# Optimization experiments

Hardware: AMD Instinct MI355X
Metric: run time of the kernel (lower is better)

Reference implementation:

```python
import jax, jax.numpy as jnp
import numpy as np

D = 512            # model size
H = 8              # num_heads
HD = D // H        # head_size = 64
WIN = 7            # num_keys (payload tokens per window)
QNB = 5            # query_nb for 'mean' aggregation
SCALE = D ** -0.5  # NOTE: torch module scales by size**-0.5, not head_size**-0.5
EPS = 1e-5


def setup_inputs() -> dict:
    key = jax.random.key(0)
    ks = jax.random.split(key, 12)
    B, M = 8, 4096
    w = lambda i: jax.random.normal(ks[i], (D, D), jnp.float32) * 0.02
    return {
        "k": jax.random.normal(ks[0], (B, M, D), jnp.float32),
        "v": jax.random.normal(ks[1], (B, M, D), jnp.float32),
        "q": jax.random.normal(ks[2], (B, M, D), jnp.float32),
        "query_len": 3584,
        "Wk": w(3), "bk": jnp.zeros((D,), jnp.float32),
        "Wv": w(4), "bv": jnp.zeros((D,), jnp.float32),
        "Wq": w(5), "bq": jnp.zeros((D,), jnp.float32),
        "ln_g": jnp.ones((D,), jnp.float32), "ln_b": jnp.zeros((D,), jnp.float32),
        "Wpq": w(6), "bpq": jnp.zeros((D,), jnp.float32),
        "Wpk": w(7), "bpk": jnp.zeros((D,), jnp.float32),
        "Wo": w(8), "bo": jnp.zeros((D,), jnp.float32),
    }


def reference(k, v, q, query_len, Wk, bk, Wv, bv, Wq, bq, ln_g, ln_b, Wpq, bpq, Wpk, bpk, Wo, bo):
    B, M, _ = k.shape
    win_num = -(-query_len // WIN)     # ceil
    per_win = M // win_num

    k = k @ Wk + bk
    v = v @ Wv + bv
    q = q @ Wq + bq

    # 'mean' query aggregation: AvgPool1d(kernel=QNB, stride=1, pad=QNB//2),
    # count_include_pad=True => always divide by QNB (zero-padded)
    qp = jnp.pad(q, ((0, 0), (QNB // 2, QNB // 2), (0, 0)))
    q = sum(qp[:, j:j + M] for j in range(QNB)) / QNB

    # ---- stage 1: DSA (local attention inside each window of per_win tokens)
    resh = lambda x: x.reshape(B, win_num, per_win, H, HD).transpose(0, 1, 3, 2, 4)
    dq, dk, dv = resh(q), resh(k), resh(v)                       # [B,W,H,p,hd]
    attn = jax.nn.softmax(jnp.einsum('bwhqd,bwhkd->bwhqk', dq, dk) * SCALE, axis=-1)
    out = jnp.einsum('bwhqk,bwhkd->bwhqd', attn, dv)
    out = out.transpose(0, 1, 3, 2, 4).reshape(B, win_num, per_win, D)

    win_tok = out[:, :, 0, :]          # [B, W, D] window summary tokens
    attn_x = out[:, :, 1:, :]

    # LayerNorm + exact GELU on window tokens
    mu = win_tok.mean(-1, keepdims=True)
    var = ((win_tok - mu) ** 2).mean(-1, keepdims=True)
    win_tok = (win_tok - mu) / jnp.sqrt(var + EPS) * ln_g + ln_b
    win_tok = jax.nn.gelu(win_tok, approximate=False)

    # ---- stage 2: PSA (attention over window summary tokens)
    pq = (win_tok @ Wpq + bpq).reshape(B, win_num, H, HD).transpose(0, 2, 1, 3)  # [B,H,W,hd]
    pk = (win_tok @ Wpk + bpk).reshape(B, win_num, H, HD).transpose(0, 2, 1, 3)
    pv = attn_x.reshape(B, win_num, WIN, H, HD).transpose(0, 3, 1, 2, 4)
    pv = pv.reshape(B, H, win_num, WIN * HD)

    pattn = jax.nn.softmax(jnp.einsum('bhqd,bhkd->bhqk', pq, pk) * SCALE, axis=-1)
    pout = jnp.einsum('bhqk,bhkd->bhqd', pattn, pv)
    pout = pout.transpose(0, 2, 1, 3).reshape(B, win_num, H, WIN, HD)
    pout = pout.transpose(0, 1, 3, 2, 4).reshape(B, win_num, WIN, D)

    out = (pout + attn_x).reshape(B, win_num * WIN, D)[:, :query_len, :]
    return out @ Wo + bo
```

## Files before the change

### kernel.cpp

```cpp
#include <hip/hip_runtime.h>
#include <hip/hip_bf16.h>
#include <math.h>

#define SCALE_ 0.04419417382415922f
#define EPS_  1e-5f

typedef unsigned short u16;
typedef __attribute__((ext_vector_type(8))) short     bf16x8;
typedef __attribute__((ext_vector_type(4))) float     f32x4;
typedef __attribute__((ext_vector_type(8))) unsigned short u16x8;
typedef __attribute__((ext_vector_type(4))) unsigned short u16x4;

__device__ __forceinline__ u16 f2b(float f) {
  union { float f; unsigned int u; } x; x.f = f;
  unsigned int u = x.u;
  return (u16)((u + 0x7FFFu + ((u >> 16) & 1u)) >> 16);
}
__device__ __forceinline__ float b2f(u16 h) {
  union { unsigned int u; float f; } x; x.u = ((unsigned int)h) << 16;
  return x.f;
}
__device__ __forceinline__ void gload_lds16(const void* g, void* l) {
  __builtin_amdgcn_global_load_lds(
      (const __attribute__((address_space(1))) void*)g,
      (__attribute__((address_space(3))) void*)l, 16, 0, 0);
}

__global__ __launch_bounds__(256) void wconv(
    const float* W0, const float* W1, const float* W2,
    const float* W3, const float* W4, const float* W5, u16* wt)
{
  const float* W;
  switch (blockIdx.z) {
    case 0: W = W0; break; case 1: W = W1; break; case 2: W = W2; break;
    case 3: W = W3; break; case 4: W = W4; break; default: W = W5; break;
  }
  u16* Wt = wt + (size_t)blockIdx.z * 262144;
  const int k0 = blockIdx.x * 64, n0 = blockIdx.y * 64;
  __shared__ float T[64][68];
  const int tid = threadIdx.x;
#pragma unroll
  for (int it = 0; it < 4; ++it) {
    int L = it * 256 + tid;
    int r = L >> 4, cg = L & 15;
    float4 v = *reinterpret_cast<const float4*>(W + (size_t)(k0 + r) * 512 + n0 + cg * 4);
    T[r][cg * 4 + 0] = v.x; T[r][cg * 4 + 1] = v.y;
    T[r][cg * 4 + 2] = v.z; T[r][cg * 4 + 3] = v.w;
  }
  __syncthreads();
#pragma unroll
  for (int it = 0; it < 2; ++it) {
    int L = it * 256 + tid;
    int rn = L >> 3, kg = L & 7;
    u16x8 o;
#pragma unroll
    for (int e = 0; e < 8; ++e) o[e] = f2b(T[kg * 8 + e][rn]);
    *(u16x8*)(Wt + (size_t)(n0 + rn) * 512 + k0 + kg * 8) = o;
  }
}

__global__ __launch_bounds__(512) void gemm_proj(
    const float* A0, const u16* Bt0, const float* bi0, u16* C0,
    const float* A1, const u16* Bt1, const float* bi1, u16* C1,
    const float* A2, const u16* Bt2, const float* bi2, u16* C2)
{
  const float *A, *bias; const u16* Bt; u16* C;
  if (blockIdx.z == 0)      { A = A0; Bt = Bt0; bias = bi0; C = C0; }
  else if (blockIdx.z == 1) { A = A1; Bt = Bt1; bias = bi1; C = C1; }
  else                      { A = A2; Bt = Bt2; bias = bi2; C = C2; }

  __shared__ u16 As[8192];
  __shared__ u16 Bs[32768];
  const int tid = threadIdx.x;
  const int lane = tid & 63, wid = tid >> 6;
  const int wr = wid >> 2, wcn = wid & 3;
  const int l15 = lane & 15, lh = lane >> 4, l7 = lane & 7;
  const int m0 = blockIdx.x * 128;

  const f32x4 fz = {0.f, 0.f, 0.f, 0.f};
  f32x4 acc[4][8];
#pragma unroll
  for (int m = 0; m < 4; ++m)
#pragma unroll
    for (int n = 0; n < 8; ++n) acc[m][n] = fz;

  int aoff[2], boff[2];
#pragma unroll
  for (int kh = 0; kh < 2; ++kh) {
    int slot = ((kh * 4 + lh) ^ l7) << 4;
    aoff[kh] = (wr * 64 + l15) * 128 + slot;
    boff[kh] = (wcn * 128 + l15) * 128 + slot;
  }

  for (int k0 = 0; k0 < 512; k0 += 64) {
    __syncthreads();
#pragma unroll
    for (int it = 0; it < 8; ++it) {
      int L = it * 512 + tid;
      int r = L >> 3, s = L & 7;
      int c = s ^ (r & 7);
      gload_lds16(Bt + (size_t)r * 512 + k0 + c * 8,
                  (char*)Bs + (it * 512 + wid * 64) * 16);
    }
    float4 xa[2], xb[2];
#pragma unroll
    for (int it = 0; it < 2; ++it) {
      int L = it * 512 + tid;
      int r = L >> 3, s = L & 7;
      int c = s ^ (r & 7);
      const float* ga = A + (size_t)(m0 + r) * 512 + k0 + c * 8;
      xa[it] = *reinterpret_cast<const float4*>(ga);
      xb[it] = *reinterpret_cast<const float4*>(ga + 4);
    }
#pragma unroll
    for (int it = 0; it < 2; ++it) {
      int L = it * 512 + tid;
      u16x8 o;
      o[0] = f2b(xa[it].x); o[1] = f2b(xa[it].y);
      o[2] = f2b(xa[it].z); o[3] = f2b(xa[it].w);
      o[4] = f2b(xb[it].x); o[5] = f2b(xb[it].y);
      o[6] = f2b(xb[it].z); o[7] = f2b(xb[it].w);
      *(u16x8*)((char*)As + L * 16) = o;
    }
    __syncthreads();
#pragma unroll
    for (int kh = 0; kh < 2; ++kh) {
      bf16x8 af[4], bfr[8];
#pragma unroll
      for (int m = 0; m < 4; ++m)
        af[m] = *(const bf16x8*)((const char*)As + aoff[kh] + m * 2048);
#pragma unroll
      for (int n = 0; n < 8; ++n)
        bfr[n] = *(const bf16x8*)((const char*)Bs + boff[kh] + n * 2048);
#pragma unroll
      for (int m = 0; m < 4; ++m)
#pragma unroll
        for (int n = 0; n < 8; ++n)
          acc[m][n] = __builtin_amdgcn_mfma_f32_16x16x32_bf16(af[m], bfr[n], acc[m][n], 0, 0, 0);
    }
  }

  const int gn0 = wcn * 128 + l15;
  float bv[8];
#pragma unroll
  for (int n = 0; n < 8; ++n) bv[n] = bias[gn0 + n * 16];
#pragma unroll
  for (int m = 0; m < 4; ++m)
#pragma unroll
    for (int reg = 0; reg < 4; ++reg) {
      int gm = m0 + wr * 64 + m * 16 + lh * 4 + reg;
#pragma unroll
      for (int n = 0; n < 8; ++n)
        C[(size_t)gm * 512 + gn0 + n * 16] = f2b(acc[m][n][reg] + bv[n]);
    }
}

__global__ __launch_bounds__(512) void gemm_out(
    const u16* __restrict__ A, const u16* __restrict__ Bt,
    const float* __restrict__ bias, float* __restrict__ C)
{
  __shared__ u16 As[8192];
  __shared__ u16 Bs[32768];
  const int tid = threadIdx.x;
  const int lane = tid & 63, wid = tid >> 6;
  const int wr = wid >> 2, wcn = wid & 3;
  const int l15 = lane & 15, lh = lane >> 4, l7 = lane & 7;
  const int m0 = blockIdx.x * 128;

  const f32x4 fz = {0.f, 0.f, 0.f, 0.f};
  f32x4 acc[4][8];
#pragma unroll
  for (int m = 0; m < 4; ++m)
#pragma unroll
    for (int n = 0; n < 8; ++n) acc[m][n] = fz;

  int aoff[2], boff[2];
#pragma unroll
  for (int kh = 0; kh < 2; ++kh) {
    int slot = ((kh * 4 + lh) ^ l7) << 4;
    aoff[kh] = (wr * 64 + l15) * 128 + slot;
    boff[kh] = (wcn * 128 + l15) * 128 + slot;
  }

  for (int k0 = 0; k0 < 512; k0 += 64) {
    __syncthreads();
#pragma unroll
    for (int it = 0; it < 8; ++it) {
      int L = it * 512 + tid;
      int r = L >> 3, s = L & 7;
      int c = s ^ (r & 7);
      gload_lds16(Bt + (size_t)r * 512 + k0 + c * 8,
                  (char*)Bs + (it * 512 + wid * 64) * 16);
    }
#pragma unroll
    for (int it = 0; it < 2; ++it) {
      int L = it * 512 + tid;
      int r = L >> 3, s = L & 7;
      int c = s ^ (r & 7);
      gload_lds16(A + (size_t)(m0 + r) * 512 + k0 + c * 8,
                  (char*)As + (it * 512 + wid * 64) * 16);
    }
    __syncthreads();
#pragma unroll
    for (int kh = 0; kh < 2; ++kh) {
      bf16x8 af[4], bfr[8];
#pragma unroll
      for (int m = 0; m < 4; ++m)
        af[m] = *(const bf16x8*)((const char*)As + aoff[kh] + m * 2048);
#pragma unroll
      for (int n = 0; n < 8; ++n)
        bfr[n] = *(const bf16x8*)((const char*)Bs + boff[kh] + n * 2048);
#pragma unroll
      for (int m = 0; m < 4; ++m)
#pragma unroll
        for (int n = 0; n < 8; ++n)
          acc[m][n] = __builtin_amdgcn_mfma_f32_16x16x32_bf16(af[m], bfr[n], acc[m][n], 0, 0, 0);
    }
  }

  const int gn0 = wcn * 128 + l15;
  float bv[8];
#pragma unroll
  for (int n = 0; n < 8; ++n) bv[n] = bias[gn0 + n * 16];
#pragma unroll
  for (int m = 0; m < 4; ++m)
#pragma unroll
    for (int reg = 0; reg < 4; ++reg) {
      int gm = m0 + wr * 64 + m * 16 + lh * 4 + reg;
#pragma unroll
      for (int n = 0; n < 8; ++n)
        C[(size_t)gm * 512 + gn0 + n * 16] = acc[m][n][reg] + bv[n];
    }
}

__global__ __launch_bounds__(256) void gemm_pp(
    const u16* __restrict__ A,
    const u16* __restrict__ Bt0, const float* __restrict__ bi0, float* __restrict__ C0,
    const u16* __restrict__ Bt1, const float* __restrict__ bi1, float* __restrict__ C1)
{
  const u16* Bt; const float* bias; float* C;
  if (blockIdx.z == 0) { Bt = Bt0; bias = bi0; C = C0; }
  else                 { Bt = Bt1; bias = bi1; C = C1; }

  __shared__ u16 As[8192];
  __shared__ u16 Bs[8192];
  const int tid = threadIdx.x;
  const int lane = tid & 63, wid = tid >> 6;
  const int wr = wid >> 1, wc = wid & 1;
  const int l15 = lane & 15, lh = lane >> 4, l7 = lane & 7;
  const int m0 = blockIdx.x * 128, n0 = blockIdx.y * 128;

  const f32x4 fz = {0.f, 0.f, 0.f, 0.f};
  f32x4 acc[4][4];
#pragma unroll
  for (int m = 0; m < 4; ++m)
#pragma unroll
    for (int n = 0; n < 4; ++n) acc[m][n] = fz;

  int aoff[2], boff[2];
#pragma unroll
  for (int kh = 0; kh < 2; ++kh) {
    int slot = ((kh * 4 + lh) ^ l7) << 4;
    aoff[kh] = (wr * 64 + l15) * 128 + slot;
    boff[kh] = (wc * 64 + l15) * 128 + slot;
  }

  for (int k0 = 0; k0 < 512; k0 += 64) {
    __syncthreads();
#pragma unroll
    for (int it = 0; it < 4; ++it) {
      int L = it * 256 + tid;
      int r = L >> 3, s = L & 7;
      int c = s ^ (r & 7);
      gload_lds16(A  + (size_t)(m0 + r) * 512 + k0 + c * 8,
                  (char*)As + (it * 256 + wid * 64) * 16);
      gload_lds16(Bt + (size_t)(n0 + r) * 512 + k0 + c * 8,
                  (char*)Bs + (it * 256 + wid * 64) * 16);
    }
    __syncthreads();
#pragma unroll
    for (int kh = 0; kh < 2; ++kh) {
      bf16x8 af[4], bfr[4];
#pragma unroll
      for (int m = 0; m < 4; ++m)
        af[m] = *(const bf16x8*)((const char*)As + aoff[kh] + m * 2048);
#pragma unroll
      for (int n = 0; n < 4; ++n)
        bfr[n] = *(const bf16x8*)((const char*)Bs + boff[kh] + n * 2048);
#pragma unroll
      for (int m = 0; m < 4; ++m)
#pragma unroll
        for (int n = 0; n < 4; ++n)
          acc[m][n] = __builtin_amdgcn_mfma_f32_16x16x32_bf16(af[m], bfr[n], acc[m][n], 0, 0, 0);
    }
  }

  const int gn0 = n0 + wc * 64 + l15;
  float bv[4];
#pragma unroll
  for (int n = 0; n < 4; ++n) bv[n] = bias[gn0 + n * 16];
#pragma unroll
  for (int m = 0; m < 4; ++m)
#pragma unroll
    for (int reg = 0; reg < 4; ++reg) {
      int gm = m0 + wr * 64 + m * 16 + lh * 4 + reg;
#pragma unroll
      for (int n = 0; n < 4; ++n)
        C[(size_t)gm * 512 + gn0 + n * 16] = acc[m][n][reg] + bv[n];
    }
}

__global__ __launch_bounds__(64) void attn_win(
    const u16* kp, const u16* vp, const u16* qp0, u16* attn)
{
  const int h = blockIdx.x, w = blockIdx.y, b = blockIdx.z;
  const int t = threadIdx.x;
  __shared__ float ks[8][68], vs[8][68], qr[12][68], qs[8][68], Ps[8][9];
  const size_t base = ((size_t)b * 4096 + (size_t)w * 8) * 512 + h * 64;

  {
    int i = t >> 3, dg = t & 7;
    u16x8 kv = *(const u16x8*)(kp + base + (size_t)i * 512 + dg * 8);
    u16x8 vv = *(const u16x8*)(vp + base + (size_t)i * 512 + dg * 8);
#pragma unroll
    for (int e = 0; e < 8; ++e) {
      ks[i][dg * 8 + e] = b2f(kv[e]);
      vs[i][dg * 8 + e] = b2f(vv[e]);
    }
  }
#pragma unroll
  for (int l = 0; l < 2; ++l) {
    int L = t + l * 64;
    if (L < 96) {
      int i = L >> 3, dg = L & 7;
      int m = w * 8 - 2 + i;
      if (m >= 0 && m < 4096) {
        u16x8 qv = *(const u16x8*)(qp0 + ((size_t)b * 4096 + m) * 512 + h * 64 + dg * 8);
#pragma unroll
        for (int e = 0; e < 8; ++e) qr[i][dg * 8 + e] = b2f(qv[e]);
      } else {
#pragma unroll
        for (int e = 0; e < 8; ++e) qr[i][dg * 8 + e] = 0.0f;
      }
    }
  }
  __syncthreads();
#pragma unroll
  for (int j = 0; j < 8; ++j)
    qs[j][t] = 0.2f * (qr[j][t] + qr[j + 1][t] + qr[j + 2][t] + qr[j + 3][t] + qr[j + 4][t]);
  __syncthreads();

  const int qi = t >> 3, kj = t & 7;
  float s = 0.0f;
#pragma unroll
  for (int d = 0; d < 64; ++d) s = fmaf(qs[qi][d], ks[kj][d], s);
  s *= SCALE_;
  float mx = s;
  mx = fmaxf(mx, __shfl_xor(mx, 1));
  mx = fmaxf(mx, __shfl_xor(mx, 2));
  mx = fmaxf(mx, __shfl_xor(mx, 4));
  float e = expf(s - mx);
  float sum = e;
  sum += __shfl_xor(sum, 1);
  sum += __shfl_xor(sum, 2);
  sum += __shfl_xor(sum, 4);
  Ps[qi][kj] = e / sum;
  __syncthreads();

  float o[8];
#pragma unroll
  for (int c = 0; c < 8; ++c) o[c] = 0.0f;
#pragma unroll
  for (int tt = 0; tt < 8; ++tt) {
    float pw = Ps[qi][tt];
#pragma unroll
    for (int c = 0; c < 8; ++c) o[c] = fmaf(pw, vs[tt][kj * 8 + c], o[c]);
  }
  u16x8 ov;
#pragma unroll
  for (int c = 0; c < 8; ++c) ov[c] = f2b(o[c]);
  *(u16x8*)(attn + base + (size_t)qi * 512 + kj * 8) = ov;
}

__global__ __launch_bounds__(256) void pvt_build(const u16* attn, u16* pvT)
{
  const int bh = blockIdx.x;
  const int b = bh >> 3, h = bh & 7;
  const int w0 = blockIdx.y * 32;
  __shared__ u16 TL[448 * 40];
  const int tid = threadIdx.x;
#pragma unroll
  for (int it = 0; it < 8; ++it) {
    int L = it * 256 + tid;
    int dg = L & 7, r = L >> 3;
    int w2l = r >> 3, tt = r & 7;
    if (tt < 7) {
      int m = 8 * (w0 + w2l) + tt + 1;
      u16x8 v = *(const u16x8*)(attn + ((size_t)b * 4096 + m) * 512 + h * 64 + dg * 8);
#pragma unroll
      for (int e = 0; e < 8; ++e)
        TL[(tt * 64 + dg * 8 + e) * 40 + w2l] = v[e];
    }
  }
  __syncthreads();
#pragma unroll
  for (int it = 0; it < 7; ++it) {
    int L = it * 256 + tid;
    int n = L >> 2, seg = L & 3;
    u16x8 v = *(const u16x8*)(&TL[n * 40 + seg * 8]);
    *(u16x8*)(pvT + ((size_t)bh * 448 + n) * 512 + w0 + seg * 8) = v;
  }
}

__global__ __launch_bounds__(64) void ln_gelu(
    const u16* attn, const float* g, const float* be, u16* wt)
{
  const int r = blockIdx.x;
  const int b = r >> 9, w = r & 511;
  const int t = threadIdx.x;
  const u16* x = attn + (((size_t)b * 4096) + (size_t)w * 8) * 512;

  u16x8 v = *(const u16x8*)(x + t * 8);
  float xv[8];
  float s1 = 0.f, s2 = 0.f;
#pragma unroll
  for (int e = 0; e < 8; ++e) {
    xv[e] = b2f(v[e]);
    s1 += xv[e]; s2 += xv[e] * xv[e];
  }
#pragma unroll
  for (int off = 1; off < 64; off <<= 1) {
    s1 += __shfl_xor(s1, off);
    s2 += __shfl_xor(s2, off);
  }
  const float mu  = s1 * (1.0f / 512.0f);
  const float var = s2 * (1.0f / 512.0f) - mu * mu;
  const float inv = 1.0f / sqrtf(var + EPS_);

  const int d0 = t * 8;
  float4 g0 = *reinterpret_cast<const float4*>(g + d0);
  float4 g1 = *reinterpret_cast<const float4*>(g + d0 + 4);
  float4 b0 = *reinterpret_cast<const float4*>(be + d0);
  float4 b1 = *reinterpret_cast<const float4*>(be + d0 + 4);
  float gv[8] = {g0.x, g0.y, g0.z, g0.w, g1.x, g1.y, g1.z, g1.w};
  float bvv[8] = {b0.x, b0.y, b0.z, b0.w, b1.x, b1.y, b1.z, b1.w};
  const float k2 = 0.70710678118654752f;
  u16x8 ov;
#pragma unroll
  for (int e = 0; e < 8; ++e) {
    float y = (xv[e] - mu) * inv * gv[e] + bvv[e];
    ov[e] = f2b(0.5f * y * (1.0f + erff(y * k2)));
  }
  *(u16x8*)(wt + (size_t)r * 512 + d0) = ov;
}

__global__ __launch_bounds__(256) void qk_exp(
    const float* pq, const float* pk, u16* expS)
{
  const int bh = blockIdx.z;
  const int b = bh >> 3, h = bh & 7;
  const int wq0 = blockIdx.x * 64, wk0 = blockIdx.y * 64;
  const int tid = threadIdx.x;

  __shared__ float Aq[64][68];
  __shared__ float Bk[64][68];

#pragma unroll
  for (int l = 0; l < 4; ++l) {
    int L = tid + l * 256;
    int row = L >> 4, dv = L & 15;
    float4 a = *reinterpret_cast<const float4*>(pq + ((size_t)b * 512 + wq0 + row) * 512 + h * 64 + dv * 4);
    float4 c = *reinterpret_cast<const float4*>(pk + ((size_t)b * 512 + wk0 + row) * 512 + h * 64 + dv * 4);
    Aq[dv * 4 + 0][row] = a.x; Aq[dv * 4 + 1][row] = a.y;
    Aq[dv * 4 + 2][row] = a.z; Aq[dv * 4 + 3][row] = a.w;
    Bk[dv * 4 + 0][row] = c.x; Bk[dv * 4 + 1][row] = c.y;
    Bk[dv * 4 + 2][row] = c.z; Bk[dv * 4 + 3][row] = c.w;
  }
  __syncthreads();

  const int r0 = (tid >> 4) * 4, c0 = (tid & 15) * 4;
  float acc[4][4];
#pragma unroll
  for (int i = 0; i < 4; ++i)
#pragma unroll
    for (int j = 0; j < 4; ++j) acc[i][j] = 0.0f;

#pragma unroll
  for (int kk = 0; kk < 64; ++kk) {
    float4 a = *reinterpret_cast<const float4*>(&Aq[kk][r0]);
    float4 c = *reinterpret_cast<const float4*>(&Bk[kk][c0]);
    float av[4] = {a.x, a.y, a.z, a.w};
    float cv[4] = {c.x, c.y, c.z, c.w};
#pragma unroll
    for (int i = 0; i < 4; ++i)
#pragma unroll
      for (int j = 0; j < 4; ++j)
        acc[i][j] = fmaf(av[i], cv[j], acc[i][j]);
  }

#pragma unroll
  for (int i = 0; i < 4; ++i) {
    u16x4 o;
#pragma unroll
    for (int j = 0; j < 4; ++j) o[j] = f2b(expf(acc[i][j] * SCALE_));
    *(u16x4*)(expS + ((size_t)bh * 512 + wq0 + r0 + i) * 512 + wk0 + c0) = o;
  }
}

__global__ __launch_bounds__(256) void rs_inv(const u16* expS, float* rsinv)
{
  const int row = blockIdx.x * 4 + (threadIdx.x >> 6);
  const int t = threadIdx.x & 63;
  u16x8 v = *(const u16x8*)(expS + (size_t)row * 512 + t * 8);
  float s = 0.f;
#pragma unroll
  for (int e = 0; e < 8; ++e) s += b2f(v[e]);
#pragma unroll
  for (int off = 1; off < 64; off <<= 1) s += __shfl_xor(s, off);
  if (t == 0) rsinv[row] = 1.0f / s;
}

__global__ __launch_bounds__(256) void pv_mfma(
    const u16* __restrict__ expS, const u16* __restrict__ pvT,
    const float* __restrict__ rsinv, const u16* __restrict__ attn,
    u16* __restrict__ X2)
{
  __shared__ u16 As[8192];
  __shared__ u16 Bs[4096];
  const int tid = threadIdx.x;
  const int lane = tid & 63, wid = tid >> 6;
  const int wr = wid >> 1, wc = wid & 1;
  const int l15 = lane & 15, lh = lane >> 4, l7 = lane & 7;
  const int bh = blockIdx.z, b = bh >> 3, h = bh & 7;
  const int m0 = blockIdx.x * 128;
  const int nt = blockIdx.y;

  const f32x4 fz = {0.f, 0.f, 0.f, 0.f};
  f32x4 acc[4][2];
#pragma unroll
  for (int m = 0; m < 4; ++m)
#pragma unroll
    for (int n = 0; n < 2; ++n) acc[m][n] = fz;

  int aoff[2], boff[2];
#pragma unroll
  for (int kh = 0; kh < 2; ++kh) {
    int slot = ((kh * 4 + lh) ^ l7) << 4;
    aoff[kh] = (wr * 64 + l15) * 128 + slot;
    boff[kh] = (wc * 32 + l15) * 128 + slot;
  }

  for (int k0 = 0; k0 < 512; k0 += 64) {
    __syncthreads();
#pragma unroll
    for (int it = 0; it < 4; ++it) {
      int L = it * 256 + tid;
      int r = L >> 3, s = L & 7;
      int c = s ^ (r & 7);
      gload_lds16(expS + ((size_t)bh * 512 + m0 + r) * 512 + k0 + c * 8,
                  (char*)As + (it * 256 + wid * 64) * 16);
    }
#pragma unroll
    for (int it = 0; it < 2; ++it) {
      int L = it * 256 + tid;
      int r = L >> 3, s = L & 7;
      int c = s ^ (r & 7);
      gload_lds16(pvT + ((size_t)bh * 448 + nt * 64 + r) * 512 + k0 + c * 8,
                  (char*)Bs + (it * 256 + wid * 64) * 16);
    }
    __syncthreads();
#pragma unroll
    for (int kh = 0; kh < 2; ++kh) {
      bf16x8 af[4], bfr[2];
#pragma unroll
      for (int m = 0; m < 4; ++m)
        af[m] = *(const bf16x8*)((const char*)As + aoff[kh] + m * 2048);
#pragma unroll
      for (int n = 0; n < 2; ++n)
        bfr[n] = *(const bf16x8*)((const char*)Bs + boff[kh] + n * 2048);
#pragma unroll
      for (int m = 0; m < 4; ++m)
#pragma unroll
        for (int n = 0; n < 2; ++n)
          acc[m][n] = __builtin_amdgcn_mfma_f32_16x16x32_bf16(af[m], bfr[n], acc[m][n], 0, 0, 0);
    }
  }

#pragma unroll
  for (int m = 0; m < 4; ++m)
#pragma unroll
    for (int reg = 0; reg < 4; ++reg) {
      int gm = m0 + wr * 64 + m * 16 + lh * 4 + reg;
      float ri = rsinv[bh * 512 + gm];
#pragma unroll
      for (int n = 0; n < 2; ++n) {
        int d = wc * 32 + n * 16 + l15;
        float res = b2f(attn[((size_t)b * 4096 + gm * 8 + nt + 1) * 512 + h * 64 + d]);
        X2[((size_t)b * 3584 + gm * 7 + nt) * 512 + h * 64 + d] =
            f2b(acc[m][n][reg] * ri + res);
      }
    }
}

extern "C" void kernel_launch(void* const* d_in, const int* in_sizes, int n_in,
                              void* d_out, int out_size, void* d_ws, size_t ws_size,
                              hipStream_t stream)
{
  const float* k_in = (const float*)d_in[0];
  const float* v_in = (const float*)d_in[1];
  const float* q_in = (const float*)d_in[2];
  const float* Wk  = (const float*)d_in[4];
  const float* bk  = (const float*)d_in[5];
  const float* Wv  = (const float*)d_in[6];
  const float* bv  = (const float*)d_in[7];
  const float* Wq  = (const float*)d_in[8];
  const float* bq  = (const float*)d_in[9];
  const float* lng = (const float*)d_in[10];
  const float* lnb = (const float*)d_in[11];
  const float* Wpq = (const float*)d_in[12];
  const float* bpq = (const float*)d_in[13];
  const float* Wpk = (const float*)d_in[14];
  const float* bpk = (const float*)d_in[15];
  const float* Wo  = (const float*)d_in[16];
  const float* bo  = (const float*)d_in[17];
  float* out = (float*)d_out;

  char* ws = (char*)d_ws;
  const size_t MB = 1024 * 1024;
  u16* wtb  = (u16*)(ws);
  u16* kp   = (u16*)(ws + 16 * MB);
  u16* vp   = (u16*)(ws + 52 * MB);
  u16* qp0  = (u16*)(ws + 88 * MB);
  u16* attn = (u16*)(ws + 124 * MB);
  u16*   wt    = (u16*)(ws + 16 * MB);
  float* pq    = (float*)(ws + 20 * MB);
  float* pk    = (float*)(ws + 28 * MB);
  float* rsinv = (float*)(ws + 36 * MB);
  u16*   expS  = (u16*)(ws + 40 * MB);
  u16*   pvT   = (u16*)(ws + 76 * MB);
  u16*   X2    = (u16*)(ws + 160 * MB);

  u16* Wkt  = wtb;
  u16* Wvt  = wtb + 1 * 262144;
  u16* Wqt  = wtb + 2 * 262144;
  u16* Wpqt = wtb + 3 * 262144;
  u16* Wpkt = wtb + 4 * 262144;
  u16* Wot  = wtb + 5 * 262144;

  wconv<<<dim3(8, 8, 6), 256, 0, stream>>>(Wk, Wv, Wq, Wpq, Wpk, Wo, wtb);

  gemm_proj<<<dim3(256, 1, 3), 512, 0, stream>>>(
      k_in, Wkt, bk, kp,
      v_in, Wvt, bv, vp,
      q_in, Wqt, bq, qp0);

  attn_win<<<dim3(8, 512, 8), 64, 0, stream>>>(kp, vp, qp0, attn);
  pvt_build<<<dim3(64, 16), 256, 0, stream>>>(attn, pvT);
  ln_gelu<<<4096, 64, 0, stream>>>(attn, lng, lnb, wt);

  gemm_pp<<<dim3(32, 4, 2), 256, 0, stream>>>(
      wt, Wpqt, bpq, pq, Wpkt, bpk, pk);

  qk_exp<<<dim3(8, 8, 64), 256, 0, stream>>>(pq, pk, expS);
  rs_inv<<<8192, 256, 0, stream>>>(expS, rsinv);
  pv_mfma<<<dim3(4, 7, 64), 256, 0, stream>>>(expS, pvT, rsinv, attn, X2);

  gemm_out<<<dim3(224, 1, 1), 512, 0, stream>>>(X2, Wot, bo, out);
}
```

Baseline: 301.3 us.

## Double-buffer projection GEMMs and move PSA QK scores onto bf16 MFMA

The projection and output GEMMs now use K-steps of 32 with two LDS buffers, so the global loads for the next step are issued before the MFMAs on the current step, and a new XOR swizzle suits the 64-byte rows. gemm_pp now writes pq and pk in bf16. The scalar fp32 qk_exp kernel is replaced by qk_mfma, which loads them with global-to-LDS copies and computes scores with bf16 MFMA. This is meant to hide memory latency in the big GEMMs and move the PSA score computation onto the matrix cores, at the cost of bf16 rounding on the query and key projections.

New measurement: 281.1 us. -6.7%, faster.

```diff
diff --git a/kernel.cpp b/kernel.cpp
--- a/kernel.cpp
+++ b/kernel.cpp
@@ -69,13 +69,17 @@
   else if (blockIdx.z == 1) { A = A1; Bt = Bt1; bias = bi1; C = C1; }
   else                      { A = A2; Bt = Bt2; bias = bi2; C = C2; }
 
-  __shared__ u16 As[8192];
-  __shared__ u16 Bs[32768];
+  __shared__ u16 As[2][4096];
+  __shared__ u16 Bs[2][16384];
   const int tid = threadIdx.x;
   const int lane = tid & 63, wid = tid >> 6;
   const int wr = wid >> 2, wcn = wid & 3;
-  const int l15 = lane & 15, lh = lane >> 4, l7 = lane & 7;
+  const int l15 = lane & 15, lh = lane >> 4;
+  const int sx = (l15 >> 1) & 3;
   const int m0 = blockIdx.x * 128;
+
+  const int rr = tid >> 2, sp = tid & 3;
+  const int ssw = sp ^ ((rr >> 1) & 3);
 
   const f32x4 fz = {0.f, 0.f, 0.f, 0.f};
   f32x4 acc[4][8];
@@ -84,60 +88,57 @@
 #pragma unroll
     for (int n = 0; n < 8; ++n) acc[m][n] = fz;
 
-  int aoff[2], boff[2];
-#pragma unroll
-  for (int kh = 0; kh < 2; ++kh) {
-    int slot = ((kh * 4 + lh) ^ l7) << 4;
-    aoff[kh] = (wr * 64 + l15) * 128 + slot;
-    boff[kh] = (wcn * 128 + l15) * 128 + slot;
-  }
-
-  for (int k0 = 0; k0 < 512; k0 += 64) {
+  const int aoff0 = (wr * 64 + l15) * 64 + ((lh ^ sx) << 4);
+  const int boff0 = (wcn * 128 + l15) * 64 + ((lh ^ sx) << 4);
+
+  {
+#pragma unroll
+    for (int it = 0; it < 4; ++it)
+      gload_lds16(Bt + (size_t)(it * 128 + rr) * 512 + ssw * 8,
+                  (char*)Bs[0] + (it * 512 + wid * 64) * 16);
+    const float* ga = A + (size_t)(m0 + rr) * 512 + ssw * 8;
+    float4 x0 = *reinterpret_cast<const float4*>(ga);
+    float4 x1 = *reinterpret_cast<const float4*>(ga + 4);
+    u16x8 o;
+    o[0] = f2b(x0.x); o[1] = f2b(x0.y); o[2] = f2b(x0.z); o[3] = f2b(x0.w);
+    o[4] = f2b(x1.x); o[5] = f2b(x1.y); o[6] = f2b(x1.z); o[7] = f2b(x1.w);
+    *(u16x8*)((char*)As[0] + tid * 16) = o;
+  }
+  __syncthreads();
+
+#pragma unroll 2
+  for (int t = 0; t < 16; ++t) {
+    const int cur = t & 1, nxt = cur ^ 1;
+    float4 x0 = {0.f,0.f,0.f,0.f}, x1 = {0.f,0.f,0.f,0.f};
+    if (t < 15) {
+      const int k0 = (t + 1) * 32;
+#pragma unroll
+      for (int it = 0; it < 4; ++it)
+        gload_lds16(Bt + (size_t)(it * 128 + rr) * 512 + k0 + ssw * 8,
+                    (char*)Bs[nxt] + (it * 512 + wid * 64) * 16);
+      const float* ga = A + (size_t)(m0 + rr) * 512 + k0 + ssw * 8;
+      x0 = *reinterpret_cast<const float4*>(ga);
+      x1 = *reinterpret_cast<const float4*>(ga + 4);
+    }
+    bf16x8 af[4], bfr[8];
+#pragma unroll
+    for (int m = 0; m < 4; ++m)
+      af[m] = *(const bf16x8*)((const char*)As[cur] + aoff0 + m * 1024);
+#pragma unroll
+    for (int n = 0; n < 8; ++n)
+      bfr[n] = *(const bf16x8*)((const char*)Bs[cur] + boff0 + n * 1024);
+#pragma unroll
+    for (int m = 0; m < 4; ++m)
+#pragma unroll
+      for (int n = 0; n < 8; ++n)
+        acc[m][n] = __builtin_amdgcn_mfma_f32_16x16x32_bf16(af[m], bfr[n], acc[m][n], 0, 0, 0);
+    if (t < 15) {
+      u16x8 o;
+      o[0] = f2b(x0.x); o[1] = f2b(x0.y); o[2] = f2b(x0.z); o[3] = f2b(x0.w);
+      o[4] = f2b(x1.x); o[5] = f2b(x1.y); o[6] = f2b(x1.z); o[7] = f2b(x1.w);
+      *(u16x8*)((char*)As[nxt] + tid * 16) = o;
+    }
     __syncthreads();
-#pragma unroll
-    for (int it = 0; it < 8; ++it) {
-      int L = it * 512 + tid;
-      int r = L >> 3, s = L & 7;
-      int c = s ^ (r & 7);
-      gload_lds16(Bt + (size_t)r * 512 + k0 + c * 8,
-                  (char*)Bs + (it * 512 + wid * 64) * 16);
-    }
-    float4 xa[2], xb[2];
-#pragma unroll
-    for (int it = 0; it < 2; ++it) {
-      int L = it * 512 + tid;
-      int r = L >> 3, s = L & 7;
-      int c = s ^ (r & 7);
-      const float* ga = A + (size_t)(m0 + r) * 512 + k0 + c * 8;
-      xa[it] = *reinterpret_cast<const float4*>(ga);
-      xb[it] = *reinterpret_cast<const float4*>(ga + 4);
-    }
-#pragma unroll
-    for (int it = 0; it < 2; ++it) {
-      int L = it * 512 + tid;
-      u16x8 o;
-      o[0] = f2b(xa[it].x); o[1] = f2b(xa[it].y);
-      o[2] = f2b(xa[it].z); o[3] = f2b(xa[it].w);
-      o[4] = f2b(xb[it].x); o[5] = f2b(xb[it].y);
-      o[6] = f2b(xb[it].z); o[7] = f2b(xb[it].w);
-      *(u16x8*)((char*)As + L * 16) = o;
-    }
-    __syncthreads();
-#pragma unroll
-    for (int kh = 0; kh < 2; ++kh) {
-      bf16x8 af[4], bfr[8];
-#pragma unroll
-      for (int m = 0; m < 4; ++m)
-        af[m] = *(const bf16x8*)((const char*)As + aoff[kh] + m * 2048);
-#pragma unroll
-      for (int n = 0; n < 8; ++n)
-        bfr[n] = *(const bf16x8*)((const char*)Bs + boff[kh] + n * 2048);
-#pragma unroll
-      for (int m = 0; m < 4; ++m)
-#pragma unroll
-        for (int n = 0; n < 8; ++n)
-          acc[m][n] = __builtin_amdgcn_mfma_f32_16x16x32_bf16(af[m], bfr[n], acc[m][n], 0, 0, 0);
-    }
   }
 
   const int gn0 = wcn * 128 + l15;
@@ -159,13 +160,16 @@
     const u16* __restrict__ A, const u16* __restrict__ Bt,
     const float* __restrict__ bias, float* __restrict__ C)
 {
-  __shared__ u16 As[8192];
-  __shared__ u16 Bs[32768];
+  __shared__ u16 As[2][4096];
+  __shared__ u16 Bs[2][16384];
   const int tid = threadIdx.x;
   const int lane = tid & 63, wid = tid >> 6;
   const int wr = wid >> 2, wcn = wid & 3;
-  const int l15 = lane & 15, lh = lane >> 4, l7 = lane & 7;
+  const int l15 = lane & 15, lh = lane >> 4;
+  const int sx = (l15 >> 1) & 3;
   const int m0 = blockIdx.x * 128;
+  const int rr = tid >> 2, sp = tid & 3;
+  const int ssw = sp ^ ((rr >> 1) & 3);
 
   const f32x4 fz = {0.f, 0.f, 0.f, 0.f};
   f32x4 acc[4][8];
@@ -174,48 +178,44 @@
 #pragma unroll
     for (int n = 0; n < 8; ++n) acc[m][n] = fz;
 
-  int aoff[2], boff[2];
-#pragma unroll
-  for (int kh = 0; kh < 2; ++kh) {
-    int slot = ((kh * 4 + lh) ^ l7) << 4;
-    aoff[kh] = (wr * 64 + l15) * 128 + slot;
-    boff[kh] = (wcn * 128 + l15) * 128 + slot;
-  }
-
-  for (int k0 = 0; k0 < 512; k0 += 64) {
+  const int aoff0 = (wr * 64 + l15) * 64 + ((lh ^ sx) << 4);
+  const int boff0 = (wcn * 128 + l15) * 64 + ((lh ^ sx) << 4);
+
+  {
+#pragma unroll
+    for (int it = 0; it < 4; ++it)
+      gload_lds16(Bt + (size_t)(it * 128 + rr) * 512 + ssw * 8,
+                  (char*)Bs[0] + (it * 512 + wid * 64) * 16);
+    gload_lds16(A + (size_t)(m0 + rr) * 512 + ssw * 8,
+                (char*)As[0] + (wid * 64) * 16);
+  }
+  __syncthreads();
+
+#pragma unroll 2
+  for (int t = 0; t < 16; ++t) {
+    const int cur = t & 1, nxt = cur ^ 1;
+    if (t < 15) {
+      const int k0 = (t + 1) * 32;
+#pragma unroll
+      for (int it = 0; it < 4; ++it)
+        gload_lds16(Bt + (size_t)(it * 128 + rr) * 512 + k0 + ssw * 8,
+                    (char*)Bs[nxt] + (it * 512 + wid * 64) * 16);
+      gload_lds16(A + (size_t)(m0 + rr) * 512 + k0 + ssw * 8,
+                  (char*)As[nxt] + (wid * 64) * 16);
+    }
+    bf16x8 af[4], bfr[8];
+#pragma unroll
+    for (int m = 0; m < 4; ++m)
+      af[m] = *(const bf16x8*)((const char*)As[cur] + aoff0 + m * 1024);
+#pragma unroll
+    for (int n = 0; n < 8; ++n)
+      bfr[n] = *(const bf16x8*)((const char*)Bs[cur] + boff0 + n * 1024);
+#pragma unroll
+    for (int m = 0; m < 4; ++m)
+#pragma unroll
+      for (int n = 0; n < 8; ++n)
+        acc[m][n] = __builtin_amdgcn_mfma_f32_16x16x32_bf16(af[m], bfr[n], acc[m][n], 0, 0, 0);
     __syncthreads();
-#pragma unroll
-    for (int it = 0; it < 8; ++it) {
-      int L = it * 512 + tid;
-      int r = L >> 3, s = L & 7;
-      int c = s ^ (r & 7);
-      gload_lds16(Bt + (size_t)r * 512 + k0 + c * 8,
-                  (char*)Bs + (it * 512 + wid * 64) * 16);
-    }
-#pragma unroll
-    for (int it = 0; it < 2; ++it) {
-      int L = it * 512 + tid;
-      int r = L >> 3, s = L & 7;
-      int c = s ^ (r & 7);
-      gload_lds16(A + (size_t)(m0 + r) * 512 + k0 + c * 8,
-                  (char*)As + (it * 512 + wid * 64) * 16);
-    }
-    __syncthreads();
-#pragma unroll
-    for (int kh = 0; kh < 2; ++kh) {
-      bf16x8 af[4], bfr[8];
-#pragma unroll
-      for (int m = 0; m < 4; ++m)
-        af[m] = *(const bf16x8*)((const char*)As + aoff[kh] + m * 2048);
-#pragma unroll
-      for (int n = 0; n < 8; ++n)
-        bfr[n] = *(const bf16x8*)((const char*)Bs + boff[kh] + n * 2048);
-#pragma unroll
-      for (int m = 0; m < 4; ++m)
-#pragma unroll
-        for (int n = 0; n < 8; ++n)
-          acc[m][n] = __builtin_amdgcn_mfma_f32_16x16x32_bf16(af[m], bfr[n], acc[m][n], 0, 0, 0);
-    }
   }
 
   const int gn0 = wcn * 128 + l15;
@@ -235,10 +235,10 @@
 
 __global__ __launch_bounds__(256) void gemm_pp(
     const u16* __restrict__ A,
-    const u16* __restrict__ Bt0, const float* __restrict__ bi0, float* __restrict__ C0,
-    const u16* __restrict__ Bt1, const float* __restrict__ bi1, float* __restrict__ C1)
-{
-  const u16* Bt; const float* bias; float* C;
+    const u16* __restrict__ Bt0, const float* __restrict__ bi0, u16* __restrict__ C0,
+    const u16* __restrict__ Bt1, const float* __restrict__ bi1, u16* __restrict__ C1)
+{
+  const u16* Bt; const float* bias; u16* C;
   if (blockIdx.z == 0) { Bt = Bt0; bias = bi0; C = C0; }
   else                 { Bt = Bt1; bias = bi1; C = C1; }
 
@@ -306,7 +306,70 @@
       int gm = m0 + wr * 64 + m * 16 + lh * 4 + reg;
 #pragma unroll
       for (int n = 0; n < 4; ++n)
-        C[(size_t)gm * 512 + gn0 + n * 16] = acc[m][n][reg] + bv[n];
+        C[(size_t)gm * 512 + gn0 + n * 16] = f2b(acc[m][n][reg] + bv[n]);
+    }
+}
+
+__global__ __launch_bounds__(256) void qk_mfma(
+    const u16* __restrict__ pq, const u16* __restrict__ pk, u16* __restrict__ expS)
+{
+  __shared__ u16 As[8192];
+  __shared__ u16 Bs[8192];
+  const int tid = threadIdx.x;
+  const int lane = tid & 63, wid = tid >> 6;
+  const int wr = wid >> 1, wc = wid & 1;
+  const int l15 = lane & 15, lh = lane >> 4, l7 = lane & 7;
+  const int bh = blockIdx.z, b = bh >> 3, h = bh & 7;
+  const int wq0 = blockIdx.x * 128, wk0 = blockIdx.y * 128;
+
+  const f32x4 fz = {0.f, 0.f, 0.f, 0.f};
+  f32x4 acc[4][4];
+#pragma unroll
+  for (int m = 0; m < 4; ++m)
+#pragma unroll
+    for (int n = 0; n < 4; ++n) acc[m][n] = fz;
+
+#pragma unroll
+  for (int it = 0; it < 4; ++it) {
+    int L = it * 256 + tid;
+    int r = L >> 3, s = L & 7;
+    int c = s ^ (r & 7);
+    gload_lds16(pq + ((size_t)b * 512 + wq0 + r) * 512 + h * 64 + c * 8,
+                (char*)As + (it * 256 + wid * 64) * 16);
+    gload_lds16(pk + ((size_t)b * 512 + wk0 + r) * 512 + h * 64 + c * 8,
+                (char*)Bs + (it * 256 + wid * 64) * 16);
+  }
+  __syncthreads();
+
+#pragma unroll
+  for (int kh = 0; kh < 2; ++kh) {
+    int slot = ((kh * 4 + lh) ^ l7) << 4;
+    int aoff = (wr * 64 + l15) * 128 + slot;
+    int boff = (wc * 64 + l15) * 128 + slot;
+    bf16x8 af[4], bfr[4];
+#pragma unroll
+    for (int m = 0; m < 4; ++m)
+      af[m] = *(const bf16x8*)((const char*)As + aoff + m * 2048);
+#pragma unroll
+    for (int n = 0; n < 4; ++n)
+      bfr[n] = *(const bf16x8*)((const char*)Bs + boff + n * 2048);
+#pragma unroll
+    for (int m = 0; m < 4; ++m)
+#pragma unroll
+      for (int n = 0; n < 4; ++n)
+        acc[m][n] = __builtin_amdgcn_mfma_f32_16x16x32_bf16(af[m], bfr[n], acc[m][n], 0, 0, 0);
+  }
+
+  const int gn0 = wk0 + wc * 64 + l15;
+#pragma unroll
+  for (int m = 0; m < 4; ++m)
+#pragma unroll
+    for (int reg = 0; reg < 4; ++reg) {
+      int gm = wq0 + wr * 64 + m * 16 + lh * 4 + reg;
+#pragma unroll
+      for (int n = 0; n < 4; ++n)
+        expS[((size_t)bh * 512 + gm) * 512 + gn0 + n * 16] =
+            f2b(expf(acc[m][n][reg] * SCALE_));
     }
 }
 
@@ -452,59 +515,6 @@
     ov[e] = f2b(0.5f * y * (1.0f + erff(y * k2)));
   }
   *(u16x8*)(wt + (size_t)r * 512 + d0) = ov;
-}
-
-__global__ __launch_bounds__(256) void qk_exp(
-    const float* pq, const float* pk, u16* expS)
-{
-  const int bh = blockIdx.z;
-  const int b = bh >> 3, h = bh & 7;
-  const int wq0 = blockIdx.x * 64, wk0 = blockIdx.y * 64;
-  const int tid = threadIdx.x;
-
-  __shared__ float Aq[64][68];
-  __shared__ float Bk[64][68];
-
-#pragma unroll
-  for (int l = 0; l < 4; ++l) {
-    int L = tid + l * 256;
-    int row = L >> 4, dv = L & 15;
-    float4 a = *reinterpret_cast<const float4*>(pq + ((size_t)b * 512 + wq0 + row) * 512 + h * 64 + dv * 4);
-    float4 c = *reinterpret_cast<const float4*>(pk + ((size_t)b * 512 + wk0 + row) * 512 + h * 64 + dv * 4);
-    Aq[dv * 4 + 0][row] = a.x; Aq[dv * 4 + 1][row] = a.y;
-    Aq[dv * 4 + 2][row] = a.z; Aq[dv * 4 + 3][row] = a.w;
-    Bk[dv * 4 + 0][row] = c.x; Bk[dv * 4 + 1][row] = c.y;
-    Bk[dv * 4 + 2][row] = c.z; Bk[dv * 4 + 3][row] = c.w;
-  }
-  __syncthreads();
-
-  const int r0 = (tid >> 4) * 4, c0 = (tid & 15) * 4;
-  float acc[4][4];
-#pragma unroll
-  for (int i = 0; i < 4; ++i)
-#pragma unroll
-    for (int j = 0; j < 4; ++j) acc[i][j] = 0.0f;
-
-#pragma unroll
-  for (int kk = 0; kk < 64; ++kk) {
-    float4 a = *reinterpret_cast<const float4*>(&Aq[kk][r0]);
-    float4 c = *reinterpret_cast<const float4*>(&Bk[kk][c0]);
-    float av[4] = {a.x, a.y, a.z, a.w};
-    float cv[4] = {c.x, c.y, c.z, c.w};
-#pragma unroll
-    for (int i = 0; i < 4; ++i)
-#pragma unroll
-      for (int j = 0; j < 4; ++j)
-        acc[i][j] = fmaf(av[i], cv[j], acc[i][j]);
-  }
-
-#pragma unroll
-  for (int i = 0; i < 4; ++i) {
-    u16x4 o;
-#pragma unroll
-    for (int j = 0; j < 4; ++j) o[j] = f2b(expf(acc[i][j] * SCALE_));
-    *(u16x4*)(expS + ((size_t)bh * 512 + wq0 + r0 + i) * 512 + wk0 + c0) = o;
-  }
 }
 
 __global__ __launch_bounds__(256) void rs_inv(const u16* expS, float* rsinv)
@@ -633,8 +643,8 @@
   u16* qp0  = (u16*)(ws + 88 * MB);
   u16* attn = (u16*)(ws + 124 * MB);
   u16*   wt    = (u16*)(ws + 16 * MB);
-  float* pq    = (float*)(ws + 20 * MB);
-  float* pk    = (float*)(ws + 28 * MB);
+  u16*   pq    = (u16*)(ws + 20 * MB);
+  u16*   pk    = (u16*)(ws + 28 * MB);
   float* rsinv = (float*)(ws + 36 * MB);
   u16*   expS  = (u16*)(ws + 40 * MB);
   u16*   pvT   = (u16*)(ws + 76 * MB);
@@ -661,7 +671,7 @@
   gemm_pp<<<dim3(32, 4, 2), 256, 0, stream>>>(
       wt, Wpqt, bpq, pq, Wpkt, bpk, pk);
 
-  qk_exp<<<dim3(8, 8, 64), 256, 0, stream>>>(pq, pk, expS);
+  qk_mfma<<<dim3(4, 4, 64), 256, 0, stream>>>(pq, pk, expS);
   rs_inv<<<8192, 256, 0, stream>>>(expS, rsinv);
   pv_mfma<<<dim3(4, 7, 64), 256, 0, stream>>>(expS, pvT, rsinv, attn, X2);
 
```
